# Optimization experiments

Measured on AMD Instinct MI355X. Metric: run time of the kernel, lower is better.

Reference implementation:

```python
import jax, jax.numpy as jnp
import numpy as np

N_GOOD = 16
NUM_TEST = 16
NUM_UNITS = 32
EPS = 1e-5


def _mlp(x, w1, b1, w2, b2):
    # Linear -> ReLU -> Linear -> ReLU
    h = jax.nn.relu(x @ w1 + b1)
    return jax.nn.relu(h @ w2 + b2)


def _ln_relu(x, g, b):
    mu = jnp.mean(x, axis=-1, keepdims=True)
    var = jnp.mean(jnp.square(x - mu), axis=-1, keepdims=True)
    return jax.nn.relu((x - mu) / jnp.sqrt(var + EPS) * g + b)


def _attend(self_out, enc):
    # self_out: [B, D], enc: [B, N, D]
    scores = jnp.einsum('bd,bnd->bn', self_out, enc) / np.float32(np.sqrt(NUM_TEST))
    attn = jax.nn.softmax(scores, axis=-1)
    return jnp.einsum('bn,bnd->bd', attn, enc)


def setup_inputs() -> dict:
    key = jax.random.key(0)
    ks = jax.random.split(key, 24)
    B = 262144
    obs_dim = 4 + (N_GOOD - 1) * 5 + N_GOOD * 3  # 127

    def lin(k, fan_in, fan_out):
        bound = 1.0 / np.sqrt(fan_in)
        kw, kb = jax.random.split(k)
        w = jax.random.uniform(kw, (fan_in, fan_out), jnp.float32, -bound, bound)
        b = jax.random.uniform(kb, (fan_out,), jnp.float32, -bound, bound)
        return w, b

    en_w1, en_b1 = lin(ks[0], 4, NUM_UNITS)
    en_w2, en_b2 = lin(ks[1], NUM_UNITS, NUM_TEST)
    oa_w1, oa_b1 = lin(ks[2], 5, NUM_UNITS)
    oa_w2, oa_b2 = lin(ks[3], NUM_UNITS, NUM_TEST)
    g_w1, g_b1 = lin(ks[4], 3, NUM_UNITS)
    g_w2, g_b2 = lin(ks[5], NUM_UNITS, NUM_TEST)
    m_w1, m_b1 = lin(ks[6], NUM_TEST * 3, NUM_UNITS)
    m_w2, m_b2 = lin(ks[7], NUM_UNITS, NUM_UNITS)
    m_w3, m_b3 = lin(ks[8], NUM_UNITS, 2)

    return {
        's_input': jax.random.normal(ks[9], (B, obs_dim), jnp.float32),
        'en_w1': en_w1, 'en_b1': en_b1, 'en_w2': en_w2, 'en_b2': en_b2,
        'oa_w1': oa_w1, 'oa_b1': oa_b1, 'oa_w2': oa_w2, 'oa_b2': oa_b2,
        'oa_g': jnp.ones((NUM_TEST,), jnp.float32), 'oa_bln': jnp.zeros((NUM_TEST,), jnp.float32),
        'g_w1': g_w1, 'g_b1': g_b1, 'g_w2': g_w2, 'g_b2': g_b2,
        'g_g': jnp.ones((NUM_TEST,), jnp.float32), 'g_bln': jnp.zeros((NUM_TEST,), jnp.float32),
        'm_w1': m_w1, 'm_b1': m_b1, 'm_w2': m_w2, 'm_b2': m_b2, 'm_w3': m_w3, 'm_b3': m_b3,
    }


def reference(s_input, en_w1, en_b1, en_w2, en_b2,
              oa_w1, oa_b1, oa_w2, oa_b2, oa_g, oa_bln,
              g_w1, g_b1, g_w2, g_b2, g_g, g_bln,
              m_w1, m_b1, m_w2, m_b2, m_w3, m_b3):
    n = N_GOOD
    B = s_input.shape[0]

    # self encoding: [B, 16]
    self_out = _mlp(s_input[:, :4], en_w1, en_b1, en_w2, en_b2)

    # other agents: width (n-1)*5 = [pos pairs | vel pairs | scalar per agent]
    og = s_input[:, 4:4 + (n - 1) * 5]
    pos = og[:, :(n - 1) * 2].reshape(B, n - 1, 2)
    vel = og[:, (n - 1) * 2:(n - 1) * 4].reshape(B, n - 1, 2)
    scal = og[:, (n - 1) * 4:(n - 1) * 5].reshape(B, n - 1, 1)
    other_in = jnp.concatenate([pos, vel, scal], axis=-1)  # [B, n-1, 5]
    other_enc = _mlp(other_in, oa_w1, oa_b1, oa_w2, oa_b2)  # [B, n-1, 16]
    other_out = _ln_relu(_attend(self_out, other_enc), oa_g, oa_bln)

    # food/goals: last n*3 cols, chunks of 3
    food_in = s_input[:, -n * 3:].reshape(B, n, 3)
    food_enc = _mlp(food_in, g_w1, g_b1, g_w2, g_b2)  # [B, n, 16]
    food_out = _ln_relu(_attend(self_out, food_enc), g_g, g_bln)

    merged = jnp.concatenate([self_out, food_out, other_out], axis=1)  # [B, 48]
    h = jax.nn.leaky_relu(merged @ m_w1 + m_b1, 0.01)
    h = jax.nn.leaky_relu(h @ m_w2 + m_b2, 0.01)
    return jnp.tanh(h @ m_w3 + m_b3)  # [B, 2]
```

## Files before the change

kernel.cpp:

```cpp
#include <hip/hip_runtime.h>


#define OBS 127
#define RSTR 200
#define ZROW (32 * RSTR)
#define WWORDS (33 * RSTR)

typedef _Float16 v8h  __attribute__((ext_vector_type(8)));
typedef _Float16 v8ha __attribute__((ext_vector_type(8), aligned(16)));
typedef float    f32x8 __attribute__((ext_vector_type(8)));
typedef float    v16f __attribute__((ext_vector_type(16)));
typedef float    f4u  __attribute__((ext_vector_type(4), aligned(4)));
typedef float    f2u  __attribute__((ext_vector_type(2), aligned(4)));
typedef unsigned ui2  __attribute__((ext_vector_type(2), aligned(8)));
typedef unsigned ui4  __attribute__((ext_vector_type(4), aligned(16)));

#define MFMA16(a, b, c) __builtin_amdgcn_mfma_f32_32x32x16_f16((a), (b), (c), 0, 0, 0)

__device__ __forceinline__ unsigned pkw(float a, float b) {
    return __builtin_bit_cast(unsigned, __builtin_amdgcn_cvt_pkrtz(a, b));
}
__device__ __forceinline__ v8h zero8h() {
    v8h z;
    #pragma unroll
    for (int j = 0; j < 8; ++j) z[j] = (_Float16)0.f;
    return z;
}
__device__ __forceinline__ v8h pk8(const v16f& d, int b) {
    ui4 u;
    u[0] = pkw(d[b],     d[b + 1]);
    u[1] = pkw(d[b + 2], d[b + 3]);
    u[2] = pkw(d[b + 4], d[b + 5]);
    u[3] = pkw(d[b + 6], d[b + 7]);
    return __builtin_bit_cast(v8h, u);
}
__device__ __forceinline__ v8h pkr8(const v16f& d, int b) {
    return __builtin_elementwise_max(pk8(d, b), zero8h());
}
__device__ __forceinline__ v8h pk8v(f32x8 v) {
    ui4 u;
    u[0] = pkw(v[0], v[1]);
    u[1] = pkw(v[2], v[3]);
    u[2] = pkw(v[4], v[5]);
    u[3] = pkw(v[6], v[7]);
    return __builtin_bit_cast(v8h, u);
}
__device__ __forceinline__ v8h lrelu8(v8h t) {
    const v8h s = t * (_Float16)0.01f;
    return __builtin_elementwise_max(t, s);
}
__device__ __forceinline__ v8h a1fragK16(const float* __restrict__ W,
                                         const float* __restrict__ b,
                                         int kin, int m, int h) {
    const int Lm = (m & ~12) | ((m & 4) << 1) | ((m & 8) >> 1);
    v8h r;
    #pragma unroll
    for (int j = 0; j < 8; ++j) {
        const int k = 8 * h + j;
        const float v = (k < kin) ? W[k * 32 + Lm] : (k == kin ? b[Lm] : 0.f);
        r[j] = (_Float16)v;
    }
    return r;
}
__device__ __forceinline__ v8h a2fragK16(const float* __restrict__ W2,
                                         int s, int m, int h) {
    v8h r;
    #pragma unroll
    for (int j = 0; j < 8; ++j)
        r[j] = (_Float16)((m < 16) ? W2[(16 * s + 8 * h + j) * 16 + m] : 0.f);
    return r;
}
__device__ __forceinline__ v8h mfragK16(const float* __restrict__ W, int ncols,
                                        int base, int m, int h, int colmax) {
    v8h r;
    #pragma unroll
    for (int j = 0; j < 8; ++j) {
        const int ch = base + (j & 3) + 8 * (j >> 2) + 4 * h;
        r[j] = (_Float16)((m < colmax) ? W[ch * ncols + m] : 0.f);
    }
    return r;
}
__device__ __forceinline__ float fast_tanh(float x) {
    x = fminf(fmaxf(x, -15.f), 15.f);
    const float ex = __expf(2.f * x);
    return (ex - 1.f) / (ex + 1.f);
}

__device__ __forceinline__ v8h ld16h(const _Float16* p) {
    return *(const v8ha*)p;
}
__device__ __forceinline__ v8h ld8h(const _Float16* p) {
    const ui2 w = *(const ui2*)p;
    ui4 u;
    u[0] = w[0]; u[1] = w[1]; u[2] = 0u; u[3] = 0u;
    return __builtin_bit_cast(v8h, u);
}

__device__ __forceinline__ void estep(v8h bf, v8h A1, v8h A2a, v8h A2b,
                                      f32x8 b2v, f32x8 stl,
                                      float& l, f32x8& o, v16f z16) {
    const v16f dH = MFMA16(A1, bf, z16);
    const v8h p0 = pkr8(dH, 0);
    const v8h p1 = pkr8(dH, 8);
    v16f c = MFMA16(A2a, p0, z16);
    c = MFMA16(A2b, p1, c);
    f32x8 e2;
    #pragma unroll
    for (int r = 0; r < 8; ++r) e2[r] = fmaxf(c[r] + b2v[r], 0.f);
    float part = 0.f;
    #pragma unroll
    for (int r = 0; r < 8; ++r) part += stl[r] * e2[r];
    part += __shfl_xor(part, 32);
    const float p = __builtin_amdgcn_exp2f(part);
    l += p;
    o += p * e2;
}

__device__ __forceinline__ v8h ln_fin(float l, f32x8 o, f32x8 gv, f32x8 blv) {
    const float rl = 1.f / l;
    f32x8 a = o * rl;
    float sum = 0.f;
    #pragma unroll
    for (int r = 0; r < 8; ++r) sum += a[r];
    sum += __shfl_xor(sum, 32);
    const float mu = sum * 0.0625f;
    a -= mu;
    float var = 0.f;
    #pragma unroll
    for (int r = 0; r < 8; ++r) var += a[r] * a[r];
    var += __shfl_xor(var, 32);
    const float inv = rsqrtf(var * 0.0625f + 1e-5f);
    f32x8 v;
    #pragma unroll
    for (int r = 0; r < 8; ++r) v[r] = fmaxf(a[r] * inv * gv[r] + blv[r], 0.f);
    return pk8v(v);
}

__global__ __launch_bounds__(256, 3)
void actor_mfma(const float* __restrict__ x,
                const float* __restrict__ en_w1, const float* __restrict__ en_b1,
                const float* __restrict__ en_w2, const float* __restrict__ en_b2,
                const float* __restrict__ oa_w1, const float* __restrict__ oa_b1,
                const float* __restrict__ oa_w2, const float* __restrict__ oa_b2,
                const float* __restrict__ oa_g,  const float* __restrict__ oa_bln,
                const float* __restrict__ g_w1,  const float* __restrict__ g_b1,
                const float* __restrict__ g_w2,  const float* __restrict__ g_b2,
                const float* __restrict__ g_g,   const float* __restrict__ g_bln,
                const float* __restrict__ m_w1,  const float* __restrict__ m_b1,
                const float* __restrict__ m_w2,  const float* __restrict__ m_b2,
                const float* __restrict__ m_w3,  const float* __restrict__ m_b3,
                float* __restrict__ out, int B)
{
    const int lane = threadIdx.x & 63, wid = threadIdx.x >> 6;
    const int n = lane & 31, h = lane >> 5;

    __shared__ __align__(16) _Float16 xs_all[4][WWORDS];
    _Float16* xs = xs_all[wid];

    const int r0 = blockIdx.x * 128 + wid * 32;
    int rows = B - r0;
    rows = rows > 32 ? 32 : (rows < 0 ? 0 : rows);

    if (lane < 24) {
        ui4 z;
        z[0] = 0u; z[1] = 0u; z[2] = 0u; z[3] = 0u;
        *(ui4*)(xs + ZROW + lane * 8) = z;
    }

    if (rows > 0) {
        const float* __restrict__ xp = x + (size_t)r0 * OBS;
        if (lane < rows) {
            const f4u v = *(const f4u*)(xp + lane * OBS);
            ui4 q;
            q[0] = pkw(v[0], v[1]);
            q[1] = pkw(v[2], v[3]);
            q[2] = pkw(1.f, 0.f);
            q[3] = 0u;
            *(ui4*)(xs + lane * RSTR) = q;
        }
        #pragma unroll
        for (int i = 0; i < 8; ++i) {
            const int t = i * 64 + lane, row = t >> 4, e = t & 15;
            if (row < rows) {
                const f4u v = *(const f4u*)(xp + row * OBS + 78 + 3 * e);
                ui2 w;
                w[0] = pkw(v[1], v[2]);
                w[1] = pkw(v[3], 1.f);
                *(ui2*)(xs + row * RSTR + 8 + 4 * e) = w;
            }
        }
        #pragma unroll
        for (int i = 0; i < 8; ++i) {
            const int t = i * 64 + lane, row = t >> 4, e = t & 15;
            if (e < 15 && row < rows) {
                const float* rp = xp + row * OBS;
                const f2u pv = *(const f2u*)(rp + 4 + 2 * e);
                const f2u vv = *(const f2u*)(rp + 34 + 2 * e);
                const float sc = rp[64 + e];
                ui4 q;
                q[0] = pkw(pv[0], pv[1]);
                q[1] = pkw(vv[0], vv[1]);
                q[2] = pkw(sc, 1.f);
                q[3] = 0u;
                *(ui4*)(xs + row * RSTR + 72 + 8 * e) = q;
            }
        }
    }

    v16f z16;
    #pragma unroll
    for (int r = 0; r < 16; ++r) z16[r] = 0.f;

    f32x8 sb2v, fb2v, ob2v;
    #pragma unroll
    for (int r = 0; r < 8; ++r) {
        const int m = (r & 3) + 8 * (r >> 2) + 4 * h;
        sb2v[r] = en_b2[m];
        fb2v[r] = g_b2[m];
        ob2v[r] = oa_b2[m];
    }

    const int rbase = h ? ZROW : n * RSTR;

    f32x8 stl;
    v8h Bs;
    {
        const v8h sA1 = a1fragK16(en_w1, en_b1, 4, n, h);
        const v8h sA2a = a2fragK16(en_w2, 0, n, h);
        const v8h sA2b = a2fragK16(en_w2, 1, n, h);
        const v8h bs = ld16h(xs + rbase);
        const v16f dS = MFMA16(sA1, bs, z16);
        v16f cS = MFMA16(sA2a, pkr8(dS, 0), z16);
        cS = MFMA16(sA2b, pkr8(dS, 8), cS);
        const float SK = 0.25f * 1.44269504088896f;
        f32x8 sv;
        #pragma unroll
        for (int r = 0; r < 8; ++r) sv[r] = fmaxf(cS[r] + sb2v[r], 0.f);
        stl = sv * SK;
        Bs = pk8v(sv);
    }

    v8h fA1 = a1fragK16(g_w1, g_b1, 3, n, h);
    v8h fA2a = a2fragK16(g_w2, 0, n, h);
    v8h fA2b = a2fragK16(g_w2, 1, n, h);
    v8h oA1 = a1fragK16(oa_w1, oa_b1, 5, n, h);
    v8h oA2a = a2fragK16(oa_w2, 0, n, h);
    v8h oA2b = a2fragK16(oa_w2, 1, n, h);

    float lf = 0.f, lo = 0.f;
    f32x8 of = 0.f, oo = 0.f;
    #pragma unroll 2
    for (int e = 0; e < 16; ++e) {
        asm volatile("" : "+v"(fA1), "+v"(fA2a), "+v"(fA2b),
                          "+v"(oA1), "+v"(oA2a), "+v"(oA2b));
        asm volatile("" : "+v"(fb2v), "+v"(ob2v), "+v"(z16));
        const v8h bfF = ld8h(xs + rbase + 8 + 4 * e);
        estep(bfF, fA1, fA2a, fA2b, fb2v, stl, lf, of, z16);
        if (e < 15) {
            const v8h bfO = ld16h(xs + rbase + 72 + 8 * e);
            estep(bfO, oA1, oA2a, oA2b, ob2v, stl, lo, oo, z16);
        }
    }

    f32x8 fgv, fblv, ogv, oblv;
    #pragma unroll
    for (int r = 0; r < 8; ++r) {
        const int m = (r & 3) + 8 * (r >> 2) + 4 * h;
        fgv[r] = g_g[m];  fblv[r] = g_bln[m];
        ogv[r] = oa_g[m]; oblv[r] = oa_bln[m];
    }
    const v8h Bf = ln_fin(lf, of, fgv, fblv);
    const v8h Bo = ln_fin(lo, oo, ogv, oblv);

    v16f m1C, m2C;
    #pragma unroll
    for (int r = 0; r < 16; ++r) {
        const int m = (r & 3) + 8 * (r >> 2) + 4 * h;
        m1C[r] = m_b1[m];
        m2C[r] = m_b2[m];
    }
    v16f m1 = MFMA16(mfragK16(m_w1, 32, 0, n, h, 32), Bs, m1C);
    m1 = MFMA16(mfragK16(m_w1, 32, 16, n, h, 32), Bf, m1);
    m1 = MFMA16(mfragK16(m_w1, 32, 32, n, h, 32), Bo, m1);
    const v8h q0 = lrelu8(pk8(m1, 0));
    const v8h q1 = lrelu8(pk8(m1, 8));
    v16f m2 = MFMA16(mfragK16(m_w2, 32, 0, n, h, 32), q0, m2C);
    m2 = MFMA16(mfragK16(m_w2, 32, 16, n, h, 32), q1, m2);
    const v8h z0 = lrelu8(pk8(m2, 0));
    const v8h z1 = lrelu8(pk8(m2, 8));
    v16f m3 = MFMA16(mfragK16(m_w3, 2, 0, n, h, 2), z0, z16);
    m3 = MFMA16(mfragK16(m_w3, 2, 16, n, h, 2), z1, m3);

    if (h == 0 && n < rows) {
        float2 res;
        res.x = fast_tanh(m3[0] + m_b3[0]);
        res.y = fast_tanh(m3[1] + m_b3[1]);
        *(float2*)(out + (size_t)(r0 + n) * 2) = res;
    }
}

extern "C" void kernel_launch(void* const* d_in, const int* in_sizes, int n_in,
                              void* d_out, int out_size, void* d_ws, size_t ws_size,
                              hipStream_t stream) {
    const int B = in_sizes[0] / OBS;
    const float* xin = (const float*)d_in[0];
    const float* en_w1 = (const float*)d_in[1];
    const float* en_b1 = (const float*)d_in[2];
    const float* en_w2 = (const float*)d_in[3];
    const float* en_b2 = (const float*)d_in[4];
    const float* oa_w1 = (const float*)d_in[5];
    const float* oa_b1 = (const float*)d_in[6];
    const float* oa_w2 = (const float*)d_in[7];
    const float* oa_b2 = (const float*)d_in[8];
    const float* oa_g  = (const float*)d_in[9];
    const float* oa_bl = (const float*)d_in[10];
    const float* g_w1  = (const float*)d_in[11];
    const float* g_b1  = (const float*)d_in[12];
    const float* g_w2  = (const float*)d_in[13];
    const float* g_b2  = (const float*)d_in[14];
    const float* g_g   = (const float*)d_in[15];
    const float* g_bl  = (const float*)d_in[16];
    const float* m_w1  = (const float*)d_in[17];
    const float* m_b1  = (const float*)d_in[18];
    const float* m_w2  = (const float*)d_in[19];
    const float* m_b2  = (const float*)d_in[20];
    const float* m_w3  = (const float*)d_in[21];
    const float* m_b3  = (const float*)d_in[22];

    const int rows_per_block = 128;
    const int grid = (B + rows_per_block - 1) / rows_per_block;
    actor_mfma<<<grid, 256, 0, stream>>>(
        xin, en_w1, en_b1, en_w2, en_b2,
        oa_w1, oa_b1, oa_w2, oa_b2, oa_g, oa_bl,
        g_w1, g_b1, g_w2, g_b2, g_g, g_bl,
        m_w1, m_b1, m_w2, m_b2, m_w3, m_b3,
        (float*)d_out, B);
}
```

Before: 310.1 us.

## Process two 32-row tiles per wave to interleave MFMA chains

Each wavefront now handles 64 batch rows as two independent 32-row MFMA tiles instead of one. Blocks shrink to two waves of 128 threads with launch bounds adjusted. The goal is more instruction-level parallelism across the dependent MFMA/exp chains and reuse of per-wave weight fragments. It raises register pressure and halves waves per block, which may reduce occupancy and latency hiding.

New measurement: 346.3 us. 1.12x slower.

```diff
diff --git a/kernel.cpp b/kernel.cpp
--- a/kernel.cpp
+++ b/kernel.cpp
@@ -3,8 +3,8 @@
 
 #define OBS 127
 #define RSTR 200
-#define ZROW (32 * RSTR)
-#define WWORDS (33 * RSTR)
+#define ZROW (64 * RSTR)
+#define WWORDS (65 * RSTR)
 
 typedef _Float16 v8h  __attribute__((ext_vector_type(8)));
 typedef _Float16 v8ha __attribute__((ext_vector_type(8), aligned(16)));
@@ -96,24 +96,35 @@
     return __builtin_bit_cast(v8h, u);
 }
 
-__device__ __forceinline__ void estep(v8h bf, v8h A1, v8h A2a, v8h A2b,
-                                      f32x8 b2v, f32x8 stl,
-                                      float& l, f32x8& o, v16f z16) {
-    const v16f dH = MFMA16(A1, bf, z16);
-    const v8h p0 = pkr8(dH, 0);
-    const v8h p1 = pkr8(dH, 8);
-    v16f c = MFMA16(A2a, p0, z16);
-    c = MFMA16(A2b, p1, c);
-    f32x8 e2;
-    #pragma unroll
-    for (int r = 0; r < 8; ++r) e2[r] = fmaxf(c[r] + b2v[r], 0.f);
-    float part = 0.f;
-    #pragma unroll
-    for (int r = 0; r < 8; ++r) part += stl[r] * e2[r];
-    part += __shfl_xor(part, 32);
-    const float p = __builtin_amdgcn_exp2f(part);
-    l += p;
-    o += p * e2;
+__device__ __forceinline__ void estep2(v8h bf0, v8h bf1,
+                                       v8h A1, v8h A2a, v8h A2b,
+                                       f32x8 b2v, f32x8 stl0, f32x8 stl1,
+                                       float& l0, f32x8& o0,
+                                       float& l1, f32x8& o1, v16f z16) {
+    const v16f dH0 = MFMA16(A1, bf0, z16);
+    const v16f dH1 = MFMA16(A1, bf1, z16);
+    const v8h p00 = pkr8(dH0, 0);
+    const v8h p01 = pkr8(dH0, 8);
+    const v8h p10 = pkr8(dH1, 0);
+    const v8h p11 = pkr8(dH1, 8);
+    v16f c0 = MFMA16(A2a, p00, z16);
+    c0 = MFMA16(A2b, p01, c0);
+    v16f c1 = MFMA16(A2a, p10, z16);
+    c1 = MFMA16(A2b, p11, c1);
+    f32x8 e20, e21;
+    #pragma unroll
+    for (int r = 0; r < 8; ++r) e20[r] = fmaxf(c0[r] + b2v[r], 0.f);
+    #pragma unroll
+    for (int r = 0; r < 8; ++r) e21[r] = fmaxf(c1[r] + b2v[r], 0.f);
+    float d0 = 0.f, d1 = 0.f;
+    #pragma unroll
+    for (int r = 0; r < 8; ++r) { d0 += stl0[r] * e20[r]; d1 += stl1[r] * e21[r]; }
+    d0 += __shfl_xor(d0, 32);
+    d1 += __shfl_xor(d1, 32);
+    const float p0 = __builtin_amdgcn_exp2f(d0);
+    const float p1 = __builtin_amdgcn_exp2f(d1);
+    l0 += p0; o0 += p0 * e20;
+    l1 += p1; o1 += p1 * e21;
 }
 
 __device__ __forceinline__ v8h ln_fin(float l, f32x8 o, f32x8 gv, f32x8 blv) {
@@ -136,7 +147,7 @@
     return pk8v(v);
 }
 
-__global__ __launch_bounds__(256, 3)
+__global__ __launch_bounds__(128, 2)
 void actor_mfma(const float* __restrict__ x,
                 const float* __restrict__ en_w1, const float* __restrict__ en_b1,
                 const float* __restrict__ en_w2, const float* __restrict__ en_b2,
@@ -154,12 +165,12 @@
     const int lane = threadIdx.x & 63, wid = threadIdx.x >> 6;
     const int n = lane & 31, h = lane >> 5;
 
-    __shared__ __align__(16) _Float16 xs_all[4][WWORDS];
+    __shared__ __align__(16) _Float16 xs_all[2][WWORDS];
     _Float16* xs = xs_all[wid];
 
-    const int r0 = blockIdx.x * 128 + wid * 32;
+    const int r0 = blockIdx.x * 128 + wid * 64;
     int rows = B - r0;
-    rows = rows > 32 ? 32 : (rows < 0 ? 0 : rows);
+    rows = rows > 64 ? 64 : (rows < 0 ? 0 : rows);
 
     if (lane < 24) {
         ui4 z;
@@ -179,7 +190,7 @@
             *(ui4*)(xs + lane * RSTR) = q;
         }
         #pragma unroll
-        for (int i = 0; i < 8; ++i) {
+        for (int i = 0; i < 16; ++i) {
             const int t = i * 64 + lane, row = t >> 4, e = t & 15;
             if (row < rows) {
                 const f4u v = *(const f4u*)(xp + row * OBS + 78 + 3 * e);
@@ -190,7 +201,7 @@
             }
         }
         #pragma unroll
-        for (int i = 0; i < 8; ++i) {
+        for (int i = 0; i < 16; ++i) {
             const int t = i * 64 + lane, row = t >> 4, e = t & 15;
             if (e < 15 && row < rows) {
                 const float* rp = xp + row * OBS;
@@ -220,24 +231,33 @@
         ob2v[r] = oa_b2[m];
     }
 
-    const int rbase = h ? ZROW : n * RSTR;
-
-    f32x8 stl;
-    v8h Bs;
+    const int rb0 = h ? ZROW : n * RSTR;
+    const int rb1 = h ? ZROW : (n + 32) * RSTR;
+
+    f32x8 stl0, stl1;
+    v8h Bs0, Bs1;
     {
         const v8h sA1 = a1fragK16(en_w1, en_b1, 4, n, h);
         const v8h sA2a = a2fragK16(en_w2, 0, n, h);
         const v8h sA2b = a2fragK16(en_w2, 1, n, h);
-        const v8h bs = ld16h(xs + rbase);
-        const v16f dS = MFMA16(sA1, bs, z16);
-        v16f cS = MFMA16(sA2a, pkr8(dS, 0), z16);
-        cS = MFMA16(sA2b, pkr8(dS, 8), cS);
+        const v8h bs0 = ld16h(xs + rb0);
+        const v8h bs1 = ld16h(xs + rb1);
+        const v16f dS0 = MFMA16(sA1, bs0, z16);
+        const v16f dS1 = MFMA16(sA1, bs1, z16);
+        v16f cS0 = MFMA16(sA2a, pkr8(dS0, 0), z16);
+        cS0 = MFMA16(sA2b, pkr8(dS0, 8), cS0);
+        v16f cS1 = MFMA16(sA2a, pkr8(dS1, 0), z16);
+        cS1 = MFMA16(sA2b, pkr8(dS1, 8), cS1);
         const float SK = 0.25f * 1.44269504088896f;
-        f32x8 sv;
+        f32x8 sv0, sv1;
         #pragma unroll
-        for (int r = 0; r < 8; ++r) sv[r] = fmaxf(cS[r] + sb2v[r], 0.f);
-        stl = sv * SK;
-        Bs = pk8v(sv);
+        for (int r = 0; r < 8; ++r) sv0[r] = fmaxf(cS0[r] + sb2v[r], 0.f);
+        #pragma unroll
+        for (int r = 0; r < 8; ++r) sv1[r] = fmaxf(cS1[r] + sb2v[r], 0.f);
+        stl0 = sv0 * SK;
+        stl1 = sv1 * SK;
+        Bs0 = pk8v(sv0);
+        Bs1 = pk8v(sv1);
     }
 
     v8h fA1 = a1fragK16(g_w1, g_b1, 3, n, h);
@@ -247,18 +267,22 @@
     v8h oA2a = a2fragK16(oa_w2, 0, n, h);
     v8h oA2b = a2fragK16(oa_w2, 1, n, h);
 
-    float lf = 0.f, lo = 0.f;
-    f32x8 of = 0.f, oo = 0.f;
+    float lf0 = 0.f, lf1 = 0.f, lo0 = 0.f, lo1 = 0.f;
+    f32x8 of0 = 0.f, of1 = 0.f, oo0 = 0.f, oo1 = 0.f;
     #pragma unroll 2
     for (int e = 0; e < 16; ++e) {
         asm volatile("" : "+v"(fA1), "+v"(fA2a), "+v"(fA2b),
                           "+v"(oA1), "+v"(oA2a), "+v"(oA2b));
         asm volatile("" : "+v"(fb2v), "+v"(ob2v), "+v"(z16));
-        const v8h bfF = ld8h(xs + rbase + 8 + 4 * e);
-        estep(bfF, fA1, fA2a, fA2b, fb2v, stl, lf, of, z16);
+        const v8h bfF0 = ld8h(xs + rb0 + 8 + 4 * e);
+        const v8h bfF1 = ld8h(xs + rb1 + 8 + 4 * e);
+        estep2(bfF0, bfF1, fA1, fA2a, fA2b, fb2v, stl0, stl1,
+               lf0, of0, lf1, of1, z16);
         if (e < 15) {
-            const v8h bfO = ld16h(xs + rbase + 72 + 8 * e);
-            estep(bfO, oA1, oA2a, oA2b, ob2v, stl, lo, oo, z16);
+            const v8h bfO0 = ld16h(xs + rb0 + 72 + 8 * e);
+            const v8h bfO1 = ld16h(xs + rb1 + 72 + 8 * e);
+            estep2(bfO0, bfO1, oA1, oA2a, oA2b, ob2v, stl0, stl1,
+                   lo0, oo0, lo1, oo1, z16);
         }
     }
 
@@ -269,8 +293,10 @@
         fgv[r] = g_g[m];  fblv[r] = g_bln[m];
         ogv[r] = oa_g[m]; oblv[r] = oa_bln[m];
     }
-    const v8h Bf = ln_fin(lf, of, fgv, fblv);
-    const v8h Bo = ln_fin(lo, oo, ogv, oblv);
+    const v8h Bf0 = ln_fin(lf0, of0, fgv, fblv);
+    const v8h Bf1 = ln_fin(lf1, of1, fgv, fblv);
+    const v8h Bo0 = ln_fin(lo0, oo0, ogv, oblv);
+    const v8h Bo1 = ln_fin(lo1, oo1, ogv, oblv);
 
     v16f m1C, m2C;
     #pragma unroll
@@ -279,23 +305,39 @@
         m1C[r] = m_b1[m];
         m2C[r] = m_b2[m];
     }
-    v16f m1 = MFMA16(mfragK16(m_w1, 32, 0, n, h, 32), Bs, m1C);
-    m1 = MFMA16(mfragK16(m_w1, 32, 16, n, h, 32), Bf, m1);
-    m1 = MFMA16(mfragK16(m_w1, 32, 32, n, h, 32), Bo, m1);
-    const v8h q0 = lrelu8(pk8(m1, 0));
-    const v8h q1 = lrelu8(pk8(m1, 8));
-    v16f m2 = MFMA16(mfragK16(m_w2, 32, 0, n, h, 32), q0, m2C);
-    m2 = MFMA16(mfragK16(m_w2, 32, 16, n, h, 32), q1, m2);
-    const v8h z0 = lrelu8(pk8(m2, 0));
-    const v8h z1 = lrelu8(pk8(m2, 8));
-    v16f m3 = MFMA16(mfragK16(m_w3, 2, 0, n, h, 2), z0, z16);
-    m3 = MFMA16(mfragK16(m_w3, 2, 16, n, h, 2), z1, m3);
+    const v8h w1a = mfragK16(m_w1, 32, 0, n, h, 32);
+    const v8h w1b = mfragK16(m_w1, 32, 16, n, h, 32);
+    const v8h w1c = mfragK16(m_w1, 32, 32, n, h, 32);
+    v16f m1a = MFMA16(w1a, Bs0, m1C);
+    m1a = MFMA16(w1b, Bf0, m1a);
+    m1a = MFMA16(w1c, Bo0, m1a);
+    v16f m1b = MFMA16(w1a, Bs1, m1C);
+    m1b = MFMA16(w1b, Bf1, m1b);
+    m1b = MFMA16(w1c, Bo1, m1b);
+    const v8h w2a = mfragK16(m_w2, 32, 0, n, h, 32);
+    const v8h w2b = mfragK16(m_w2, 32, 16, n, h, 32);
+    v16f m2a = MFMA16(w2a, lrelu8(pk8(m1a, 0)), m2C);
+    m2a = MFMA16(w2b, lrelu8(pk8(m1a, 8)), m2a);
+    v16f m2b = MFMA16(w2a, lrelu8(pk8(m1b, 0)), m2C);
+    m2b = MFMA16(w2b, lrelu8(pk8(m1b, 8)), m2b);
+    const v8h w3a = mfragK16(m_w3, 2, 0, n, h, 2);
+    const v8h w3b = mfragK16(m_w3, 2, 16, n, h, 2);
+    v16f m3a = MFMA16(w3a, lrelu8(pk8(m2a, 0)), z16);
+    m3a = MFMA16(w3b, lrelu8(pk8(m2a, 8)), m3a);
+    v16f m3b = MFMA16(w3a, lrelu8(pk8(m2b, 0)), z16);
+    m3b = MFMA16(w3b, lrelu8(pk8(m2b, 8)), m3b);
 
     if (h == 0 && n < rows) {
         float2 res;
-        res.x = fast_tanh(m3[0] + m_b3[0]);
-        res.y = fast_tanh(m3[1] + m_b3[1]);
+        res.x = fast_tanh(m3a[0] + m_b3[0]);
+        res.y = fast_tanh(m3a[1] + m_b3[1]);
         *(float2*)(out + (size_t)(r0 + n) * 2) = res;
+    }
+    if (h == 0 && 32 + n < rows) {
+        float2 res;
+        res.x = fast_tanh(m3b[0] + m_b3[0]);
+        res.y = fast_tanh(m3b[1] + m_b3[1]);
+        *(float2*)(out + (size_t)(r0 + 32 + n) * 2) = res;
     }
 }
 
@@ -329,7 +371,7 @@
 
     const int rows_per_block = 128;
     const int grid = (B + rows_per_block - 1) / rows_per_block;
-    actor_mfma<<<grid, 256, 0, stream>>>(
+    actor_mfma<<<grid, 128, 0, stream>>>(
         xin, en_w1, en_b1, en_w2, en_b2,
         oa_w1, oa_b1, oa_w2, oa_b2, oa_g, oa_bl,
         g_w1, g_b1, g_w2, g_b2, g_g, g_bl,
```
